# Kernel optimization log

Hardware: AMD Instinct MI355X
Metric: run time of the kernel (lower is better)

Reference implementation:

```python
import jax, jax.numpy as jnp
import numpy as np

EPS = 1e-5  # InstanceNorm2d default eps


def setup_inputs() -> dict:
    key = jax.random.key(0)
    k1, k2, k3, k4, k5, k6 = jax.random.split(key, 6)
    B, N, C, KV, H = 8, 4096, 512, 960, 4
    dq, dk = C // 4, KV // 4
    emb1 = jax.random.normal(k1, (B, N, C), dtype=jnp.float32)
    emb_all = jax.random.normal(k2, (B, N, KV), dtype=jnp.float32)
    # per-head query Linear weights (torch Linear weight is [out, in]); 4 distinct heads
    Wq = jax.random.normal(k3, (H, dq, dq), dtype=jnp.float32) * 0.05
    # key/value: the original forward only ever uses key[0] / value[0]
    Wk = jax.random.normal(k4, (dk, dk), dtype=jnp.float32) * 0.05
    Wv = jax.random.normal(k5, (dk, dk), dtype=jnp.float32) * 0.05
    Wo = jax.random.normal(k6, (C, C), dtype=jnp.float32) * 0.05
    return {"emb1": emb1, "emb_all": emb_all, "Wq": Wq, "Wk": Wk, "Wv": Wv, "Wo": Wo}


def reference(emb1, emb_all, Wq, Wk, Wv, Wo):
    B, N, C = emb1.shape
    KV = emb_all.shape[2]
    dq, dk = C // 4, KV // 4
    # split emb1 into 4 chunks along channels -> [B, N, 4, dq], apply per-head query Linear
    Qc = emb1.reshape(B, N, 4, dq)
    Q = jnp.einsum("bnhd,hed->bhne", Qc, Wq)            # [B,4,N,dq]
    # all 4 K and V chunks use key[0]/value[0] (as in the source)
    Kc = emb_all.reshape(B, N, 4, dk)
    K = jnp.einsum("bnhd,ed->bhne", Kc, Wk)             # [B,4,N,dk]
    V = jnp.einsum("bnhd,ed->bhne", Kc, Wv)             # [B,4,N,dk]
    # channel attention: contract over tokens N -> scores [B,4,dq,dk]
    scores = jnp.einsum("bhnc,bhnk->bhck", Q, K) / jnp.sqrt(jnp.float32(KV))
    # InstanceNorm2d (no affine): normalize each (b, head) score map over (dq, dk)
    mu = scores.mean(axis=(2, 3), keepdims=True)
    var = scores.var(axis=(2, 3), keepdims=True)        # biased variance, matches torch
    normed = (scores - mu) * jax.lax.rsqrt(var + EPS)
    probs = jax.nn.softmax(normed, axis=3)              # softmax over dk
    # dropout is identity in eval mode
    context = jnp.einsum("bhck,bhnk->bhcn", probs, V)   # [B,4,dq,N]
    # permute(0,3,2,1) -> [B,N,dq,4], flatten last two -> [B,N,C]
    context = jnp.transpose(context, (0, 3, 2, 1)).reshape(B, N, C)
    O1 = jnp.einsum("bnc,ec->bne", context, Wo)         # out Linear, no bias
    return O1
```

## Files before the change

kernel.cpp:

```cpp
#include <hip/hip_runtime.h>
#include <cstdint>
#include <cstddef>

#define B_ 8
#define N_ 4096
#define C_ 512
#define KV_ 960
#define DQ 128
#define DK 240
#define NSPLIT 8

typedef __attribute__((ext_vector_type(8))) short bf16x8;
typedef __attribute__((ext_vector_type(4))) float f32x4;
#define AS1 __attribute__((address_space(1)))
#define AS3 __attribute__((address_space(3)))

__device__ __forceinline__ ushort f2bf(float f) {
  uint32_t u = __float_as_uint(f);
  u += 0x7FFFu + ((u >> 16) & 1u);
  return (ushort)(u >> 16);
}

__device__ __forceinline__ uint32_t cvtpk(float lo, float hi) {
  uint32_t r;
  asm("v_cvt_pk_bf16_f32 %0, %1, %2" : "=v"(r) : "v"(lo), "v"(hi));
  return r;
}

union bfpack {
  uint32_t u[4];
  ushort s[8];
  bf16x8 v;
};

__global__ __launch_bounds__(512) void k1_mfma(const float* __restrict__ emb1,
                                               const ushort* __restrict__ embaBF,
                                               float* __restrict__ P) {
  __shared__ ushort As[128 * 64];
  __shared__ ushort Bs[128 * 64];
  const int bh = blockIdx.x;
  const int split = blockIdx.y;
  const int jh = blockIdx.z;
  const int b = bh >> 2, h = bh & 3;
  const int t = threadIdx.x;
  const int w = t >> 6, l = t & 63;
  const int wm = w >> 1, wn = w & 1;

  const float* Abase = emb1 + (size_t)b * N_ * C_ + h * DQ;
  const ushort* Bbase = embaBF + (size_t)b * N_ * KV_;

  const int cA = t & 127;
  const int jB = t & 127;
  const int nb0 = t >> 7;
  int jl = jh * 128 + jB;
  if (jl > DK - 1) jl = DK - 1;
  const int jg = h * DK + jl;

  f32x4 acc[2][4];
#pragma unroll
  for (int fm = 0; fm < 2; ++fm)
#pragma unroll
    for (int fn = 0; fn < 4; ++fn) acc[fm][fn] = (f32x4){0.f, 0.f, 0.f, 0.f};

  const int n0 = split * (N_ / NSPLIT);
  const int lrow = l & 15;
  const int KS = (N_ / NSPLIT) / 64;

  float va[2][8];
  ushort ub[2][8];

#pragma unroll
  for (int q = 0; q < 2; ++q) {
    const float* g = Abase + (size_t)(n0 + (nb0 + q * 4) * 8) * C_ + cA;
#pragma unroll
    for (int kk = 0; kk < 8; ++kk) va[q][kk] = g[(size_t)kk * C_];
  }
#pragma unroll
  for (int q = 0; q < 2; ++q) {
    const ushort* g = Bbase + (size_t)(n0 + (nb0 + q * 4) * 8) * KV_ + jg;
#pragma unroll
    for (int kk = 0; kk < 8; ++kk) ub[q][kk] = g[(size_t)kk * KV_];
  }

  for (int ks = 0; ks < KS; ++ks) {
    bfpack pa[2], pb[2];
#pragma unroll
    for (int q = 0; q < 2; ++q)
#pragma unroll
      for (int p = 0; p < 4; ++p) pa[q].u[p] = cvtpk(va[q][2 * p], va[q][2 * p + 1]);
#pragma unroll
    for (int q = 0; q < 2; ++q)
#pragma unroll
      for (int kk = 0; kk < 8; ++kk) pb[q].s[kk] = ub[q][kk];

    __builtin_amdgcn_s_barrier();

#pragma unroll
    for (int q = 0; q < 2; ++q) {
      const int nb = nb0 + q * 4;
      *(bf16x8*)(As + cA * 64 + ((nb ^ (cA & 7)) << 3)) = pa[q].v;
      *(bf16x8*)(Bs + jB * 64 + ((nb ^ (jB & 7)) << 3)) = pb[q].v;
    }

    if (ks + 1 < KS) {
      const int nb1 = n0 + (ks + 1) * 64;
#pragma unroll
      for (int q = 0; q < 2; ++q) {
        const float* g = Abase + (size_t)(nb1 + (nb0 + q * 4) * 8) * C_ + cA;
#pragma unroll
        for (int kk = 0; kk < 8; ++kk) va[q][kk] = g[(size_t)kk * C_];
      }
#pragma unroll
      for (int q = 0; q < 2; ++q) {
        const ushort* g = Bbase + (size_t)(nb1 + (nb0 + q * 4) * 8) * KV_ + jg;
#pragma unroll
        for (int kk = 0; kk < 8; ++kk) ub[q][kk] = g[(size_t)kk * KV_];
      }
    }

    asm volatile("s_waitcnt lgkmcnt(0)" ::: "memory");
    __builtin_amdgcn_sched_barrier(0);
    __builtin_amdgcn_s_barrier();

#pragma unroll
    for (int half = 0; half < 2; ++half) {
      const int kb = half * 4 + (l >> 4);
      bf16x8 af[2], bv[4];
#pragma unroll
      for (int fm = 0; fm < 2; ++fm) {
        const int i = wm * 32 + fm * 16 + lrow;
        af[fm] = *(const bf16x8*)(As + i * 64 + ((kb ^ (i & 7)) << 3));
      }
#pragma unroll
      for (int fn = 0; fn < 4; ++fn) {
        const int j = wn * 64 + fn * 16 + lrow;
        bv[fn] = *(const bf16x8*)(Bs + j * 64 + ((kb ^ (j & 7)) << 3));
      }
#pragma unroll
      for (int fm = 0; fm < 2; ++fm)
#pragma unroll
        for (int fn = 0; fn < 4; ++fn)
          acc[fm][fn] = __builtin_amdgcn_mfma_f32_16x16x32_bf16(af[fm], bv[fn],
                                                                acc[fm][fn], 0, 0, 0);
    }
  }
  f32x4* Pv4 = (f32x4*)P + ((size_t)(split * 32 + bh) * 2 + jh) * 4096;
#pragma unroll
  for (int fm = 0; fm < 2; ++fm)
#pragma unroll
    for (int fn = 0; fn < 4; ++fn) Pv4[(fm * 4 + fn) * 512 + t] = acc[fm][fn];
}

__global__ __launch_bounds__(256) void k_reduce_frag(const f32x4* __restrict__ P,
                                                     float* __restrict__ S) {
  const int bh = blockIdx.x;
  const int g = blockIdx.y * 256 + threadIdx.x;
  const int jh = g >> 12;
  const int rest = g & 4095;
  f32x4 a = P[((size_t)bh * 2 + jh) * 4096 + rest];
#pragma unroll
  for (int s = 1; s < NSPLIT; ++s) {
    f32x4 v = P[((size_t)(s * 32 + bh) * 2 + jh) * 4096 + rest];
    a.x += v.x; a.y += v.y; a.z += v.z; a.w += v.w;
  }
  const int v = rest >> 9, tt = rest & 511;
  const int fm = v >> 2, fn = v & 3;
  const int wv = tt >> 6, l = tt & 63;
  const int wm = wv >> 1, wn = wv & 1;
  const int i0 = wm * 32 + fm * 16 + (l >> 4) * 4;
  const int j = jh * 128 + wn * 64 + fn * 16 + (l & 15);
  if (j < DK) {
    float* sp = S + (size_t)bh * (DQ * DK) + (size_t)i0 * DK + j;
    sp[0] = a.x; sp[DK] = a.y; sp[2 * DK] = a.z; sp[3 * DK] = a.w;
  }
}

__global__ __launch_bounds__(256) void k_cvt(const float4* __restrict__ in,
                                             ushort4* __restrict__ out, int n4) {
  int i = blockIdx.x * 256 + threadIdx.x;
  if (i >= n4) return;
  float4 v = in[i];
  ushort4 o;
  o.x = f2bf(v.x); o.y = f2bf(v.y); o.z = f2bf(v.z); o.w = f2bf(v.w);
  out[i] = o;
}


__global__ __launch_bounds__(256) void k_g1(const float* __restrict__ Wq,
                                            const float* __restrict__ S,
                                            float* __restrict__ U) {
  const int h = blockIdx.x, c0 = blockIdx.y * 64;
  const int b = blockIdx.z / 5, n0 = (blockIdx.z % 5) * 48;
  const float* A = Wq + (size_t)h * 16384;
  const float* Bp = S + (size_t)(b * 4 + h) * 30720 + n0;
  float* Cp = U + (size_t)(b * 4 + h) * 30720 + n0;
  __shared__ float Ast[16][65];
  __shared__ float Bst[16][49];
  const int t = threadIdx.x;
  const int mi = (t >> 4) * 4, nj = (t & 15) * 3;
  float acc[4][3] = {};
  for (int k0 = 0; k0 < 128; k0 += 16) {
    __syncthreads();
#pragma unroll
    for (int q = 0; q < 4; ++q) {
      int idx = t + q * 256, m = idx >> 4, k = idx & 15;
      Ast[k][m] = A[(size_t)(c0 + m) * 128 + k0 + k];
    }
#pragma unroll
    for (int q = 0; q < 3; ++q) {
      int idx = t + q * 256, k = idx / 48, n = idx % 48;
      Bst[k][n] = Bp[(size_t)(k0 + k) * 240 + n];
    }
    __syncthreads();
#pragma unroll
    for (int kk = 0; kk < 16; ++kk) {
      float a4[4], b3[3];
#pragma unroll
      for (int x = 0; x < 4; ++x) a4[x] = Ast[kk][mi + x];
#pragma unroll
      for (int y = 0; y < 3; ++y) b3[y] = Bst[kk][nj + y];
#pragma unroll
      for (int x = 0; x < 4; ++x)
#pragma unroll
        for (int y = 0; y < 3; ++y) acc[x][y] = fmaf(a4[x], b3[y], acc[x][y]);
    }
  }
#pragma unroll
  for (int x = 0; x < 4; ++x)
#pragma unroll
    for (int y = 0; y < 3; ++y)
      Cp[(size_t)(c0 + mi + x) * 240 + nj + y] = acc[x][y];
}

__global__ __launch_bounds__(256) void k_g2(const float* __restrict__ U,
                                            const float* __restrict__ Wk,
                                            float* __restrict__ SC) {
  const int m0 = blockIdx.x * 64, n0 = blockIdx.y * 48;
  __shared__ float Ast[16][65];
  __shared__ float Bst2[48][17];
  const int t = threadIdx.x;
  const int mi = (t >> 4) * 4, nj = (t & 15) * 3;
  float acc[4][3] = {};
  for (int k0 = 0; k0 < 240; k0 += 16) {
    __syncthreads();
#pragma unroll
    for (int q = 0; q < 4; ++q) {
      int idx = t + q * 256, m = idx >> 4, k = idx & 15;
      Ast[k][m] = U[(size_t)(m0 + m) * 240 + k0 + k];
    }
#pragma unroll
    for (int q = 0; q < 3; ++q) {
      int idx = t + q * 256, n = idx >> 4, kd = idx & 15;
      Bst2[n][kd] = Wk[(size_t)(n0 + n) * 240 + k0 + kd];
    }
    __syncthreads();
#pragma unroll
    for (int kk = 0; kk < 16; ++kk) {
      float a4[4], b3[3];
#pragma unroll
      for (int x = 0; x < 4; ++x) a4[x] = Ast[kk][mi + x];
#pragma unroll
      for (int y = 0; y < 3; ++y) b3[y] = Bst2[nj + y][kk];
#pragma unroll
      for (int x = 0; x < 4; ++x)
#pragma unroll
        for (int y = 0; y < 3; ++y) acc[x][y] = fmaf(a4[x], b3[y], acc[x][y]);
    }
  }
  const float scale = 0.0322748612183951f;
#pragma unroll
  for (int x = 0; x < 4; ++x)
#pragma unroll
    for (int y = 0; y < 3; ++y)
      SC[(size_t)(m0 + mi + x) * 240 + n0 + nj + y] = acc[x][y] * scale;
}

__global__ __launch_bounds__(256) void k_g3(const float* __restrict__ PR,
                                            const float* __restrict__ Wv,
                                            float* __restrict__ T) {
  const int m0 = blockIdx.x * 64, n0 = blockIdx.y * 48;
  __shared__ float Ast[16][65];
  __shared__ float Bst[16][49];
  const int t = threadIdx.x;
  const int mi = (t >> 4) * 4, nj = (t & 15) * 3;
  float acc[4][3] = {};
  for (int k0 = 0; k0 < 240; k0 += 16) {
    __syncthreads();
#pragma unroll
    for (int q = 0; q < 4; ++q) {
      int idx = t + q * 256, m = idx >> 4, k = idx & 15;
      Ast[k][m] = PR[(size_t)(m0 + m) * 240 + k0 + k];
    }
#pragma unroll
    for (int q = 0; q < 3; ++q) {
      int idx = t + q * 256, k = idx / 48, n = idx % 48;
      Bst[k][n] = Wv[(size_t)(k0 + k) * 240 + n0 + n];
    }
    __syncthreads();
#pragma unroll
    for (int kk = 0; kk < 16; ++kk) {
      float a4[4], b3[3];
#pragma unroll
      for (int x = 0; x < 4; ++x) a4[x] = Ast[kk][mi + x];
#pragma unroll
      for (int y = 0; y < 3; ++y) b3[y] = Bst[kk][nj + y];
#pragma unroll
      for (int x = 0; x < 4; ++x)
#pragma unroll
        for (int y = 0; y < 3; ++y) acc[x][y] = fmaf(a4[x], b3[y], acc[x][y]);
    }
  }
#pragma unroll
  for (int x = 0; x < 4; ++x)
#pragma unroll
    for (int y = 0; y < 3; ++y)
      T[(size_t)(m0 + mi + x) * 240 + n0 + nj + y] = acc[x][y];
}

__global__ __launch_bounds__(256) void k_g4(const float* __restrict__ Wo,
                                            const float* __restrict__ T,
                                            ushort* __restrict__ W3bf) {
  const int h = blockIdx.x, e0 = blockIdx.y * 64;
  const int b = blockIdx.z / 5, n0 = (blockIdx.z % 5) * 48;
  const float* Bp = T + (size_t)(b * 4 + h) * 30720 + n0;
  ushort* Cp = W3bf + (size_t)b * 491520 + h * 240 + n0;
  __shared__ float Ast[16][65];
  __shared__ float Bst[16][49];
  const int t = threadIdx.x;
  const int mi = (t >> 4) * 4, nj = (t & 15) * 3;
  float acc[4][3] = {};
  for (int k0 = 0; k0 < 128; k0 += 16) {
    __syncthreads();
#pragma unroll
    for (int q = 0; q < 4; ++q) {
      int idx = t + q * 256, m = idx >> 4, k = idx & 15;
      Ast[k][m] = Wo[(size_t)(e0 + m) * 512 + 4 * (k0 + k) + h];
    }
#pragma unroll
    for (int q = 0; q < 3; ++q) {
      int idx = t + q * 256, k = idx / 48, n = idx % 48;
      Bst[k][n] = Bp[(size_t)(k0 + k) * 240 + n];
    }
    __syncthreads();
#pragma unroll
    for (int kk = 0; kk < 16; ++kk) {
      float a4[4], b3[3];
#pragma unroll
      for (int x = 0; x < 4; ++x) a4[x] = Ast[kk][mi + x];
#pragma unroll
      for (int y = 0; y < 3; ++y) b3[y] = Bst[kk][nj + y];
#pragma unroll
      for (int x = 0; x < 4; ++x)
#pragma unroll
        for (int y = 0; y < 3; ++y) acc[x][y] = fmaf(a4[x], b3[y], acc[x][y]);
    }
  }
#pragma unroll
  for (int x = 0; x < 4; ++x)
#pragma unroll
    for (int y = 0; y < 3; ++y)
      Cp[(size_t)(e0 + mi + x) * 960 + nj + y] = f2bf(acc[x][y]);
}

__global__ __launch_bounds__(1024) void k_stats(const float* __restrict__ SC,
                                                float* __restrict__ stats) {
  const int bh = blockIdx.x;
  const float* s = SC + (size_t)bh * 30720;
  const int t = threadIdx.x;
  float sum = 0.f, sq = 0.f;
  for (int i = t; i < 30720; i += 1024) {
    float v = s[i];
    sum += v;
    sq = fmaf(v, v, sq);
  }
#pragma unroll
  for (int o = 32; o > 0; o >>= 1) {
    sum += __shfl_down(sum, o);
    sq += __shfl_down(sq, o);
  }
  __shared__ float s1[16], s2[16];
  if ((t & 63) == 0) { s1[t >> 6] = sum; s2[t >> 6] = sq; }
  __syncthreads();
  if (t == 0) {
    float ts = 0.f, tq = 0.f;
#pragma unroll
    for (int i = 0; i < 16; ++i) { ts += s1[i]; tq += s2[i]; }
    const float mu = ts * (1.f / 30720.f);
    const float var = tq * (1.f / 30720.f) - mu * mu;
    stats[bh * 2] = mu;
    stats[bh * 2 + 1] = rsqrtf(var + 1e-5f);
  }
}

__global__ __launch_bounds__(512) void k_softmax(const float* __restrict__ SC,
                                                 const float* __restrict__ stats,
                                                 float* __restrict__ PR) {
  const int bh = blockIdx.x;
  const float mu = stats[bh * 2], rstd = stats[bh * 2 + 1];
  const int wv = threadIdx.x >> 6, l = threadIdx.x & 63;
  const int row0 = blockIdx.y * 32 + wv * 4;
  const float* s = SC + (size_t)bh * 30720;
  float* p = PR + (size_t)bh * 30720;
#pragma unroll
  for (int r = 0; r < 4; ++r) {
    const float* srow = s + (size_t)(row0 + r) * 240;
    float* prow = p + (size_t)(row0 + r) * 240;
    float x0 = (srow[l] - mu) * rstd;
    float x1 = (srow[64 + l] - mu) * rstd;
    float x2 = (srow[128 + l] - mu) * rstd;
    float x3 = (l < 48) ? (srow[192 + l] - mu) * rstd : -1e30f;
    float m = fmaxf(fmaxf(x0, x1), fmaxf(x2, x3));
#pragma unroll
    for (int o = 32; o > 0; o >>= 1) m = fmaxf(m, __shfl_xor(m, o));
    float e0 = __expf(x0 - m), e1 = __expf(x1 - m), e2 = __expf(x2 - m);
    float e3 = (l < 48) ? __expf(x3 - m) : 0.f;
    float ss = e0 + e1 + e2 + e3;
#pragma unroll
    for (int o = 32; o > 0; o >>= 1) ss += __shfl_xor(ss, o);
    const float inv = 1.f / ss;
    prow[l] = e0 * inv;
    prow[64 + l] = e1 * inv;
    prow[128 + l] = e2 * inv;
    if (l < 48) prow[192 + l] = e3 * inv;
  }
}

__global__ __launch_bounds__(256) void k3_mfma(const ushort* __restrict__ A,
                                               const ushort* __restrict__ Bw,
                                               float* __restrict__ C) {
  __shared__ ushort As[128 * 32];
  __shared__ ushort Bs[128 * 32];
  const int bid = blockIdx.x;
  const int swz = (bid & 7) * 128 + (bid >> 3);
  const int b = swz >> 7;
  const int rem = swz & 127;
  const int mt = rem >> 2, nt = rem & 3;
  const int t = threadIdx.x;
  const int w = t >> 6, l = t & 63;
  const int wr = w >> 1, wc = w & 1;

  const ushort* Ab = A + (size_t)b * N_ * KV_ + (size_t)mt * 128 * KV_;
  const ushort* Bb = Bw + (size_t)b * C_ * KV_ + (size_t)nt * 128 * KV_;

  const int r_l = l >> 2;
  const int c_l = (l & 3) * 8;

  f32x4 acc[4][4];
#pragma unroll
  for (int fm = 0; fm < 4; ++fm)
#pragma unroll
    for (int fn = 0; fn < 4; ++fn) acc[fm][fn] = (f32x4){0.f, 0.f, 0.f, 0.f};

  const int lrow = l & 15;
  const int lk = (l >> 4) * 8;

  for (int k0 = 0; k0 < KV_; k0 += 32) {
#pragma unroll
    for (int inst = 0; inst < 2; ++inst) {
      const int gi = w * 2 + inst;
      const ushort* ga = Ab + (size_t)(gi * 16 + r_l) * KV_ + k0 + c_l;
      __builtin_amdgcn_global_load_lds((AS1 const uint32_t*)(uintptr_t)ga,
                                       (AS3 uint32_t*)(uintptr_t)(As + gi * 512),
                                       16, 0, 0);
      const ushort* gb = Bb + (size_t)(gi * 16 + r_l) * KV_ + k0 + c_l;
      __builtin_amdgcn_global_load_lds((AS1 const uint32_t*)(uintptr_t)gb,
                                       (AS3 uint32_t*)(uintptr_t)(Bs + gi * 512),
                                       16, 0, 0);
    }
    __syncthreads();
    bf16x8 af[4], bfr[4];
#pragma unroll
    for (int fm = 0; fm < 4; ++fm)
      af[fm] = *(const bf16x8*)(As + (wr * 64 + fm * 16 + lrow) * 32 + lk);
#pragma unroll
    for (int fn = 0; fn < 4; ++fn)
      bfr[fn] = *(const bf16x8*)(Bs + (wc * 64 + fn * 16 + lrow) * 32 + lk);
#pragma unroll
    for (int fm = 0; fm < 4; ++fm)
#pragma unroll
      for (int fn = 0; fn < 4; ++fn)
        acc[fm][fn] = __builtin_amdgcn_mfma_f32_16x16x32_bf16(af[fm], bfr[fn],
                                                              acc[fm][fn], 0, 0, 0);
    __syncthreads();
  }

  float* Cb = C + (size_t)b * N_ * C_ + ((size_t)mt * 128) * C_ + nt * 128;
  const int col = wc * 64 + (l & 15);
  const int rbase = wr * 64 + (l >> 4) * 4;
#pragma unroll
  for (int fm = 0; fm < 4; ++fm)
#pragma unroll
    for (int fn = 0; fn < 4; ++fn)
#pragma unroll
      for (int r = 0; r < 4; ++r)
        Cb[(size_t)(rbase + fm * 16 + r) * C_ + col + fn * 16] = acc[fm][fn][r];
}

extern "C" void kernel_launch(void* const* d_in, const int* in_sizes, int n_in,
                              void* d_out, int out_size, void* d_ws, size_t ws_size,
                              hipStream_t stream) {
  const float* emb1 = (const float*)d_in[0];
  const float* emba = (const float*)d_in[1];
  const float* Wq   = (const float*)d_in[2];
  const float* Wk   = (const float*)d_in[3];
  const float* Wv   = (const float*)d_in[4];
  const float* Wo   = (const float*)d_in[5];
  float* out = (float*)d_out;
  char* ws = (char*)d_ws;

  ushort* embaBF = (ushort*)(ws);
  float*  S      = (float*)(ws + 62914560);
  float*  T      = (float*)(ws + 62914560);
  float*  U      = (float*)(ws + 66846720);
  ushort* W3bf   = (ushort*)(ws + 66846720);
  float*  SCb    = (float*)(ws + 70778880);
  float*  PRb    = (float*)(ws + 74711040);
  float*  P      = out;
  float*  stats  = (float*)((char*)d_out + 41943040);

  k_cvt<<<30720, 256, 0, stream>>>((const float4*)emba, (ushort4*)embaBF, 7864320);

  k1_mfma<<<dim3(32, NSPLIT, 2), 512, 0, stream>>>(emb1, embaBF, P);
  k_reduce_frag<<<dim3(32, 32), 256, 0, stream>>>((const f32x4*)P, S);

  k_g1<<<dim3(4, 2, 40), 256, 0, stream>>>(Wq, S, U);
  k_g2<<<dim3(64, 5), 256, 0, stream>>>(U, Wk, SCb);
  k_stats<<<32, 1024, 0, stream>>>(SCb, stats);
  k_softmax<<<dim3(32, 4), 512, 0, stream>>>(SCb, stats, PRb);
  k_g3<<<dim3(64, 5), 256, 0, stream>>>(PRb, Wv, T);
  k_g4<<<dim3(4, 8, 40), 256, 0, stream>>>(Wo, T, W3bf);

  k3_mfma<<<1024, 256, 0, stream>>>(embaBF, W3bf, out);
}
```

Before: 243.6 us.

## Rewrite scores GEMM with pre-converted bf16 inputs, direct-to-LDS loads, and transpose reads

A separate kernel now converts emb1 to bf16, and the N-contraction GEMM is rewritten to stage both operands with global_load_lds into double-buffered LDS. Fragments are read with ds_read_b64_tr_b16 transposing loads. Each block now covers the full 256-wide DK range (4x4 fragments per wave) instead of splitting it into two halves, which removes the duplicated A loads and the strided per-element global reads. The cost is an extra conversion pass over emb1 and new scratch placement, with stats moved into the workspace and emb1BF placed in the output buffer.

```diff
diff --git a/kernel.cpp b/kernel.cpp
--- a/kernel.cpp
+++ b/kernel.cpp
@@ -12,6 +12,7 @@
 
 typedef __attribute__((ext_vector_type(8))) short bf16x8;
 typedef __attribute__((ext_vector_type(4))) float f32x4;
+typedef __attribute__((ext_vector_type(2))) unsigned int u32x2;
 #define AS1 __attribute__((address_space(1)))
 #define AS3 __attribute__((address_space(3)))
 
@@ -21,159 +22,17 @@
   return (ushort)(u >> 16);
 }
 
-__device__ __forceinline__ uint32_t cvtpk(float lo, float hi) {
-  uint32_t r;
-  asm("v_cvt_pk_bf16_f32 %0, %1, %2" : "=v"(r) : "v"(lo), "v"(hi));
-  return r;
-}
-
-union bfpack {
-  uint32_t u[4];
-  ushort s[8];
+union frag_u {
+  u32x2 p[2];
   bf16x8 v;
 };
 
-__global__ __launch_bounds__(512) void k1_mfma(const float* __restrict__ emb1,
-                                               const ushort* __restrict__ embaBF,
-                                               float* __restrict__ P) {
-  __shared__ ushort As[128 * 64];
-  __shared__ ushort Bs[128 * 64];
-  const int bh = blockIdx.x;
-  const int split = blockIdx.y;
-  const int jh = blockIdx.z;
-  const int b = bh >> 2, h = bh & 3;
-  const int t = threadIdx.x;
-  const int w = t >> 6, l = t & 63;
-  const int wm = w >> 1, wn = w & 1;
-
-  const float* Abase = emb1 + (size_t)b * N_ * C_ + h * DQ;
-  const ushort* Bbase = embaBF + (size_t)b * N_ * KV_;
-
-  const int cA = t & 127;
-  const int jB = t & 127;
-  const int nb0 = t >> 7;
-  int jl = jh * 128 + jB;
-  if (jl > DK - 1) jl = DK - 1;
-  const int jg = h * DK + jl;
-
-  f32x4 acc[2][4];
-#pragma unroll
-  for (int fm = 0; fm < 2; ++fm)
-#pragma unroll
-    for (int fn = 0; fn < 4; ++fn) acc[fm][fn] = (f32x4){0.f, 0.f, 0.f, 0.f};
-
-  const int n0 = split * (N_ / NSPLIT);
-  const int lrow = l & 15;
-  const int KS = (N_ / NSPLIT) / 64;
-
-  float va[2][8];
-  ushort ub[2][8];
-
-#pragma unroll
-  for (int q = 0; q < 2; ++q) {
-    const float* g = Abase + (size_t)(n0 + (nb0 + q * 4) * 8) * C_ + cA;
-#pragma unroll
-    for (int kk = 0; kk < 8; ++kk) va[q][kk] = g[(size_t)kk * C_];
-  }
-#pragma unroll
-  for (int q = 0; q < 2; ++q) {
-    const ushort* g = Bbase + (size_t)(n0 + (nb0 + q * 4) * 8) * KV_ + jg;
-#pragma unroll
-    for (int kk = 0; kk < 8; ++kk) ub[q][kk] = g[(size_t)kk * KV_];
-  }
-
-  for (int ks = 0; ks < KS; ++ks) {
-    bfpack pa[2], pb[2];
-#pragma unroll
-    for (int q = 0; q < 2; ++q)
-#pragma unroll
-      for (int p = 0; p < 4; ++p) pa[q].u[p] = cvtpk(va[q][2 * p], va[q][2 * p + 1]);
-#pragma unroll
-    for (int q = 0; q < 2; ++q)
-#pragma unroll
-      for (int kk = 0; kk < 8; ++kk) pb[q].s[kk] = ub[q][kk];
-
-    __builtin_amdgcn_s_barrier();
-
-#pragma unroll
-    for (int q = 0; q < 2; ++q) {
-      const int nb = nb0 + q * 4;
-      *(bf16x8*)(As + cA * 64 + ((nb ^ (cA & 7)) << 3)) = pa[q].v;
-      *(bf16x8*)(Bs + jB * 64 + ((nb ^ (jB & 7)) << 3)) = pb[q].v;
-    }
-
-    if (ks + 1 < KS) {
-      const int nb1 = n0 + (ks + 1) * 64;
-#pragma unroll
-      for (int q = 0; q < 2; ++q) {
-        const float* g = Abase + (size_t)(nb1 + (nb0 + q * 4) * 8) * C_ + cA;
-#pragma unroll
-        for (int kk = 0; kk < 8; ++kk) va[q][kk] = g[(size_t)kk * C_];
-      }
-#pragma unroll
-      for (int q = 0; q < 2; ++q) {
-        const ushort* g = Bbase + (size_t)(nb1 + (nb0 + q * 4) * 8) * KV_ + jg;
-#pragma unroll
-        for (int kk = 0; kk < 8; ++kk) ub[q][kk] = g[(size_t)kk * KV_];
-      }
-    }
-
-    asm volatile("s_waitcnt lgkmcnt(0)" ::: "memory");
-    __builtin_amdgcn_sched_barrier(0);
-    __builtin_amdgcn_s_barrier();
-
-#pragma unroll
-    for (int half = 0; half < 2; ++half) {
-      const int kb = half * 4 + (l >> 4);
-      bf16x8 af[2], bv[4];
-#pragma unroll
-      for (int fm = 0; fm < 2; ++fm) {
-        const int i = wm * 32 + fm * 16 + lrow;
-        af[fm] = *(const bf16x8*)(As + i * 64 + ((kb ^ (i & 7)) << 3));
-      }
-#pragma unroll
-      for (int fn = 0; fn < 4; ++fn) {
-        const int j = wn * 64 + fn * 16 + lrow;
-        bv[fn] = *(const bf16x8*)(Bs + j * 64 + ((kb ^ (j & 7)) << 3));
-      }
-#pragma unroll
-      for (int fm = 0; fm < 2; ++fm)
-#pragma unroll
-        for (int fn = 0; fn < 4; ++fn)
-          acc[fm][fn] = __builtin_amdgcn_mfma_f32_16x16x32_bf16(af[fm], bv[fn],
-                                                                acc[fm][fn], 0, 0, 0);
-    }
-  }
-  f32x4* Pv4 = (f32x4*)P + ((size_t)(split * 32 + bh) * 2 + jh) * 4096;
-#pragma unroll
-  for (int fm = 0; fm < 2; ++fm)
-#pragma unroll
-    for (int fn = 0; fn < 4; ++fn) Pv4[(fm * 4 + fn) * 512 + t] = acc[fm][fn];
-}
-
-__global__ __launch_bounds__(256) void k_reduce_frag(const f32x4* __restrict__ P,
-                                                     float* __restrict__ S) {
-  const int bh = blockIdx.x;
-  const int g = blockIdx.y * 256 + threadIdx.x;
-  const int jh = g >> 12;
-  const int rest = g & 4095;
-  f32x4 a = P[((size_t)bh * 2 + jh) * 4096 + rest];
-#pragma unroll
-  for (int s = 1; s < NSPLIT; ++s) {
-    f32x4 v = P[((size_t)(s * 32 + bh) * 2 + jh) * 4096 + rest];
-    a.x += v.x; a.y += v.y; a.z += v.z; a.w += v.w;
-  }
-  const int v = rest >> 9, tt = rest & 511;
-  const int fm = v >> 2, fn = v & 3;
-  const int wv = tt >> 6, l = tt & 63;
-  const int wm = wv >> 1, wn = wv & 1;
-  const int i0 = wm * 32 + fm * 16 + (l >> 4) * 4;
-  const int j = jh * 128 + wn * 64 + fn * 16 + (l & 15);
-  if (j < DK) {
-    float* sp = S + (size_t)bh * (DQ * DK) + (size_t)i0 * DK + j;
-    sp[0] = a.x; sp[DK] = a.y; sp[2 * DK] = a.z; sp[3 * DK] = a.w;
-  }
-}
+#define S_(x) #x
+#define SX(x) S_(x)
+#define TR8(dst, base, imm) \
+  asm volatile("ds_read_b64_tr_b16 %0, %1 offset:" SX(imm) : "=v"(dst) : "v"(base))
+#define LDFRAG(dst, base, i1, i2) \
+  { frag_u f_; TR8(f_.p[0], base, i1); TR8(f_.p[1], base, i2); dst = f_.v; }
 
 __global__ __launch_bounds__(256) void k_cvt(const float4* __restrict__ in,
                                              ushort4* __restrict__ out, int n4) {
@@ -185,6 +44,139 @@
   out[i] = o;
 }
 
+__global__ __launch_bounds__(512) void k1_mfma(const ushort* __restrict__ emb1BF,
+                                               const ushort* __restrict__ embaBF,
+                                               float* __restrict__ P) {
+  __shared__ ushort LDS_[2][24576];
+  const int bh = blockIdx.x;
+  const int split = blockIdx.y;
+  const int b = bh >> 2, h = bh & 3;
+  const int t = threadIdx.x;
+  const int w = t >> 6, l = t & 63;
+  const int wr = w >> 2, wn = w & 3;
+  const int n0 = split * (N_ / NSPLIT);
+
+  const ushort* srcA[2];
+#pragma unroll
+  for (int q = 0; q < 2; ++q) {
+    uint byte = w * 2048 + q * 1024 + (l << 4);
+    uint s = byte >> 7, inner = byte & 127;
+    uint jr = inner >> 5, i0 = (inner & 31) >> 1;
+    uint g = s & 3, par = (s >> 2) & 1, fmv = (s >> 3) & 7, kv = s >> 6;
+    uint noff = kv * 32 + g * 8 + par * 4 + jr;
+    srcA[q] = emb1BF + (size_t)b * (N_ * C_) + (size_t)(n0 + noff) * C_ +
+              h * DQ + fmv * 16 + i0;
+  }
+  const ushort* srcB[4];
+#pragma unroll
+  for (int q = 0; q < 4; ++q) {
+    uint byte = w * 4096 + q * 1024 + (l << 4);
+    uint s = byte >> 7, inner = byte & 127;
+    uint jr = inner >> 5, i0 = (inner & 31) >> 1;
+    uint g = s & 3, par = (s >> 2) & 1, jbv = (s >> 3) & 15, kv = s >> 7;
+    uint noff = kv * 32 + g * 8 + par * 4 + jr;
+    srcB[q] = embaBF + (size_t)b * (N_ * KV_) + (size_t)(n0 + noff) * KV_ +
+              h * DK + jbv * 16 + i0;
+  }
+
+#define STAGE(tile, bf)                                                        \
+  do {                                                                         \
+    const size_t nadv = (size_t)(tile) * 64;                                   \
+    _Pragma("unroll") for (int q = 0; q < 2; ++q)                              \
+        __builtin_amdgcn_global_load_lds(                                      \
+            (AS1 const uint32_t*)(uintptr_t)(srcA[q] + nadv * C_),             \
+            (AS3 uint32_t*)(uintptr_t)&LDS_[bf][w * 1024 + q * 512], 16, 0, 0);\
+    _Pragma("unroll") for (int q = 0; q < 4; ++q)                              \
+        __builtin_amdgcn_global_load_lds(                                      \
+            (AS1 const uint32_t*)(uintptr_t)(srcB[q] + nadv * KV_),            \
+            (AS3 uint32_t*)(uintptr_t)&LDS_[bf][8192 + w * 2048 + q * 512],    \
+            16, 0, 0);                                                         \
+  } while (0)
+
+  f32x4 acc[4][4];
+#pragma unroll
+  for (int fm = 0; fm < 4; ++fm)
+#pragma unroll
+    for (int fn = 0; fn < 4; ++fn) acc[fm][fn] = (f32x4){0.f, 0.f, 0.f, 0.f};
+
+  const uint ldsbase = (uint)(size_t)&LDS_[0][0];
+  const uint laneoff = (uint)(l << 3);
+
+#define MMALL()                                                                \
+  asm volatile("s_waitcnt lgkmcnt(0)" ::: "memory");                           \
+  __builtin_amdgcn_sched_barrier(0);                                           \
+  _Pragma("unroll") for (int fm = 0; fm < 4; ++fm)                             \
+      _Pragma("unroll") for (int fn = 0; fn < 4; ++fn)                         \
+      acc[fm][fn] = __builtin_amdgcn_mfma_f32_16x16x32_bf16(                   \
+          af[fm], bv[fn], acc[fm][fn], 0, 0, 0)
+
+  STAGE(0, 0);
+  asm volatile("s_waitcnt vmcnt(0)" ::: "memory");
+  __builtin_amdgcn_s_barrier();
+
+  for (int ks = 0; ks < 8; ++ks) {
+    const int buf = ks & 1;
+    if (ks + 1 < 8) STAGE(ks + 1, buf ^ 1);
+    const uint aA = ldsbase + (uint)buf * 49152 + (uint)wr * 4096 + laneoff;
+    const uint aB = ldsbase + (uint)buf * 49152 + 16384 + (uint)wn * 4096 + laneoff;
+    {
+      bf16x8 af[4], bv[4];
+      LDFRAG(af[0], aA, 0, 512);
+      LDFRAG(af[1], aA, 1024, 1536);
+      LDFRAG(af[2], aA, 2048, 2560);
+      LDFRAG(af[3], aA, 3072, 3584);
+      LDFRAG(bv[0], aB, 0, 512);
+      LDFRAG(bv[1], aB, 1024, 1536);
+      LDFRAG(bv[2], aB, 2048, 2560);
+      LDFRAG(bv[3], aB, 3072, 3584);
+      MMALL();
+    }
+    {
+      bf16x8 af[4], bv[4];
+      LDFRAG(af[0], aA, 8192, 8704);
+      LDFRAG(af[1], aA, 9216, 9728);
+      LDFRAG(af[2], aA, 10240, 10752);
+      LDFRAG(af[3], aA, 11264, 11776);
+      LDFRAG(bv[0], aB, 16384, 16896);
+      LDFRAG(bv[1], aB, 17408, 17920);
+      LDFRAG(bv[2], aB, 18432, 18944);
+      LDFRAG(bv[3], aB, 19456, 19968);
+      MMALL();
+    }
+    asm volatile("s_waitcnt vmcnt(0)" ::: "memory");
+    __builtin_amdgcn_s_barrier();
+  }
+#undef STAGE
+#undef MMALL
+
+  f32x4* Pv4 = (f32x4*)P + (size_t)(split * 32 + bh) * 8192;
+#pragma unroll
+  for (int fm = 0; fm < 4; ++fm)
+#pragma unroll
+    for (int fn = 0; fn < 4; ++fn) Pv4[(fm * 4 + fn) * 512 + t] = acc[fm][fn];
+}
+
+__global__ __launch_bounds__(256) void k_reduce_frag(const f32x4* __restrict__ P,
+                                                     float* __restrict__ S) {
+  const int bh = blockIdx.x;
+  const int g = blockIdx.y * 256 + threadIdx.x;
+  f32x4 a = P[(size_t)bh * 8192 + g];
+#pragma unroll
+  for (int s = 1; s < NSPLIT; ++s) {
+    f32x4 v = P[(size_t)s * 262144 + (size_t)bh * 8192 + g];
+    a.x += v.x; a.y += v.y; a.z += v.z; a.w += v.w;
+  }
+  const int v = g >> 9, tt = g & 511;
+  const int fm = v >> 2, fn = v & 3;
+  const int wv = tt >> 6, l = tt & 63;
+  const int wr = wv >> 2, wc = wv & 3;
+  const int i0 = wr * 64 + fm * 16 + (l >> 4) * 4;
+  const int j = wc * 64 + fn * 16 + (l & 15);
+  if (j < DK) {
+    float* sp = S + (size_t)bh * (DQ * DK) + (size_t)i0 * DK + j;
+    sp[0] = a.x; sp[DK] = a.y; sp[2 * DK] = a.z; sp[3 * DK] = a.w;
+  }
+}
 
 __global__ __launch_bounds__(256) void k_g1(const float* __restrict__ Wq,
                                             const float* __restrict__ S,
@@ -516,11 +508,13 @@
   float*  SCb    = (float*)(ws + 70778880);
   float*  PRb    = (float*)(ws + 74711040);
   float*  P      = out;
-  float*  stats  = (float*)((char*)d_out + 41943040);
-
+  ushort* emb1BF = (ushort*)((char*)d_out + 33554432);
+  float*  stats  = (float*)(ws + 66846720);
+
+  k_cvt<<<16384, 256, 0, stream>>>((const float4*)emb1, (ushort4*)emb1BF, 4194304);
   k_cvt<<<30720, 256, 0, stream>>>((const float4*)emba, (ushort4*)embaBF, 7864320);
 
-  k1_mfma<<<dim3(32, NSPLIT, 2), 512, 0, stream>>>(emb1, embaBF, P);
+  k1_mfma<<<dim3(32, NSPLIT), 512, 0, stream>>>(emb1BF, embaBF, P);
   k_reduce_frag<<<dim3(32, 32), 256, 0, stream>>>((const f32x4*)P, S);
 
   k_g1<<<dim3(4, 2, 40), 256, 0, stream>>>(Wq, S, U);
```

After: 249.2 us. 1.02x slower.
